# Kernel tuning notes

Hardware: AMD Instinct MI355X
Metric: run time of the kernel (lower is better)

## Reference

```python
import jax, jax.numpy as jnp
import numpy as np

# E2M1 (FP4) value table: low 3 bits magnitude, bit 3 sign (indices 8..15 negative)
FP4_TABLE = jnp.array([0.0, 0.5, 1.0, 1.5, 2.0, 3.0, 4.0, 6.0,
                       0.0, -0.5, -1.0, -1.5, -2.0, -3.0, -4.0, -6.0], dtype=jnp.float32)
FP4_BLOCK = 32  # per-row 1x32 scale groups


def dequant_fp4(packed, scale):
    """packed: [E, O, I//2] uint8 (two e2m1 nibbles per byte, low nibble first),
    scale: [E, O, I//32] float32 (e8m0, i.e. powers of two). Returns [E, O, I] float32."""
    lo = (packed & 15).astype(jnp.int32)
    hi = ((packed >> 4) & 15).astype(jnp.int32)
    # interleave low, high nibbles along the input dim (matches torch stack(...,-1).flatten)
    vals = FP4_TABLE[jnp.stack([lo, hi], axis=-1)]  # [E, O, I//2, 2]
    w = vals.reshape(packed.shape[0], packed.shape[1], packed.shape[2] * 2)
    return w * jnp.repeat(scale, FP4_BLOCK, axis=-1)


def setup_inputs() -> dict:
    T, H, F, E, K = 2048, 2048, 1024, 16, 4
    key = jax.random.key(0)
    k = jax.random.split(key, 8)
    hidden_states = jax.random.normal(k[0], (T, H), dtype=jnp.float32)
    topk_weights = jax.nn.softmax(jax.random.normal(k[1], (T, K)), axis=-1)
    topk_ids = jax.random.randint(k[2], (T, K), 0, E, dtype=jnp.int32)
    # checkpoint-native packed FP4 expert weights + e8m0 (power-of-two) scales
    gate_up_weight = jax.random.randint(k[3], (E, 2 * F, H // 2), 0, 256, dtype=jnp.int32).astype(jnp.uint8)
    gate_up_scale = jnp.exp2(jax.random.randint(k[4], (E, 2 * F, H // 32), -8, -5).astype(jnp.float32))
    down_weight = jax.random.randint(k[5], (E, H, F // 2), 0, 256, dtype=jnp.int32).astype(jnp.uint8)
    down_scale = jnp.exp2(jax.random.randint(k[6], (E, H, F // 32), -8, -5).astype(jnp.float32))
    return {"hidden_states": hidden_states, "topk_weights": topk_weights, "topk_ids": topk_ids,
            "gate_up_weight": gate_up_weight, "gate_up_scale": gate_up_scale,
            "down_weight": down_weight, "down_scale": down_scale}


def reference(hidden_states, topk_weights, topk_ids, gate_up_weight, gate_up_scale, down_weight, down_scale):
    # 1. dequantize checkpoint-native FP4 experts to dense float weights
    w_gate_up = dequant_fp4(gate_up_weight, gate_up_scale)  # [E, 2F, H]
    w_down = dequant_fp4(down_weight, down_scale)           # [E, H, F]
    T = hidden_states.shape[0]
    E = w_gate_up.shape[0]
    # 2. scatter routing weights into a dense [T, E] combine matrix
    combine = jnp.zeros((T, E), dtype=hidden_states.dtype)
    combine = combine.at[jnp.arange(T)[:, None], topk_ids].add(topk_weights)
    # 3. grouped expert GEMM (exact dense dispatch over experts)
    gu = jnp.einsum('th,eoh->teo', hidden_states, w_gate_up)  # [T, E, 2F]
    gate, up = jnp.split(gu, 2, axis=-1)                       # gate = first ffn_dim rows
    act = jax.nn.silu(gate) * up                               # SwiGLU (swiglu_limit=0 -> no clamping)
    act = act * combine[:, :, None]                            # fold routing weights into activations
    return jnp.einsum('tef,ehf->th', act, w_down)              # [T, H]
```

## Files before the change

### kernel.cpp

```cpp
#include <hip/hip_runtime.h>
#include <stdint.h>

#define HD 2048
#define FD 1024
#define NE 16
#define NPAIR 8192
#define BM 256
#define MAXT 48
#define LDK 40

typedef short bf16x8 __attribute__((ext_vector_type(8)));
typedef float f32x4 __attribute__((ext_vector_type(4)));
typedef unsigned short u16;

static __device__ __forceinline__ u16 f2bf(float f) {
  uint32_t u = __float_as_uint(f);
  u += 0x7FFFu + ((u >> 16) & 1u);
  return (u16)(u >> 16);
}

struct DqTab { uint32_t hA, hB, lA, lB; };

static __device__ __forceinline__ DqTab make_tab(uint32_t sbits) {
  int n = (int)(sbits >> 23) - 127;
  int q = n >> 1;
  uint32_t r = (uint32_t)(n & 1);
  uint32_t mq = (uint32_t)(-q);
  uint32_t sub1 = mq * 0x01010100u;
  uint32_t subA = mq * 0x01010101u;
  DqTab t;
  t.hA = (r ? 0x40403F00u : 0x3F3F3F00u) - sub1;
  t.hB = (r ? 0x41414040u : 0x40404040u) - subA;
  t.lA = r ? 0x40008000u : 0xC0800000u;
  t.lB = r ? 0x4000C080u : 0xC0804000u;
  return t;
}

static __device__ __forceinline__ void dq8(uint32_t p, const DqTab& t, uint32_t* d) {
  uint32_t a = p & 0x0F0F0F0Fu;
  uint32_t b = (p >> 4) & 0x0F0F0F0Fu;
  uint32_t x0 = __builtin_amdgcn_perm(b, a, 0x05010400u);
  uint32_t x1 = __builtin_amdgcn_perm(b, a, 0x07030602u);
  uint32_t m0 = x0 & 0x07070707u;
  uint32_t m1 = x1 & 0x07070707u;
  uint32_t h0 = __builtin_amdgcn_perm(t.hB, t.hA, m0) | ((x0 & 0x08080808u) << 4);
  uint32_t h1 = __builtin_amdgcn_perm(t.hB, t.hA, m1) | ((x1 & 0x08080808u) << 4);
  uint32_t l0 = __builtin_amdgcn_perm(t.lB, t.lA, m0);
  uint32_t l1 = __builtin_amdgcn_perm(t.lB, t.lA, m1);
  d[0] = __builtin_amdgcn_perm(h0, l0, 0x05010400u);
  d[1] = __builtin_amdgcn_perm(h0, l0, 0x07030602u);
  d[2] = __builtin_amdgcn_perm(h1, l1, 0x05010400u);
  d[3] = __builtin_amdgcn_perm(h1, l1, 0x07030602u);
}

static __device__ __forceinline__ uint32_t pack4(int4 v) {
  return (uint32_t)(v.x & 0xFF) | ((uint32_t)(v.y & 0xFF) << 8) |
         ((uint32_t)(v.z & 0xFF) << 16) | ((uint32_t)v.w << 24);
}

static __device__ __forceinline__ bf16x8 dqfrag(const uint32_t* pB, const uint32_t* pS,
                                                int row, int kkloc, int q) {
  uint32_t pb = pB[row * 17 + kkloc * 4 + q];
  DqTab t = make_tab(pS[row * 4 + kkloc]);
  uint32_t d[4];
  dq8(pb, t, d);
  union { uint32_t u[4]; bf16x8 v; } cv;
  cv.u[0] = d[0]; cv.u[1] = d[1]; cv.u[2] = d[2]; cv.u[3] = d[3];
  return cv.v;
}

__global__ void cast_kernel(const float* __restrict__ x, u16* __restrict__ xb) {
  int i = blockIdx.x * 256 + threadIdx.x;
  float4 v = ((const float4*)x)[i];
  ushort4 o;
  o.x = f2bf(v.x); o.y = f2bf(v.y); o.z = f2bf(v.z); o.w = f2bf(v.w);
  ((ushort4*)xb)[i] = o;
}

__global__ void zero_kernel(float4* __restrict__ out) {
  out[blockIdx.x * 256 + threadIdx.x] = float4{0.f, 0.f, 0.f, 0.f};
}

__global__ void route_kernel(const int* __restrict__ ids, const float* __restrict__ tw,
                             int* __restrict__ rows, float* __restrict__ rw,
                             int* __restrict__ te, int* __restrict__ pidx) {
  __shared__ int cnt[NE], base[NE], run[NE];
  int tid = threadIdx.x;
  if (tid < NE) { cnt[tid] = 0; run[tid] = 0; }
  __syncthreads();
  for (int i = tid; i < NPAIR; i += 256) atomicAdd(&cnt[ids[i]], 1);
  __syncthreads();
  if (tid == 0) {
    int cum = 0;
    for (int e = 0; e < NE; ++e) {
      base[e] = cum;
      int nt = (cnt[e] + BM - 1) >> 8;
      for (int j = 0; j < nt; ++j) te[(cum >> 8) + j] = e;
      cum += nt << 8;
    }
    for (int t = cum >> 8; t < MAXT; ++t) te[t] = -1;
  }
  __syncthreads();
  for (int i = tid; i < MAXT * BM; i += 256) {
    rows[i] = -1;
    rw[i] = 0.f;
    if (pidx) pidx[i] = -1;
  }
  __syncthreads();
  for (int i = tid; i < NPAIR; i += 256) {
    int e = ids[i];
    int p = base[e] + atomicAdd(&run[e], 1);
    rows[p] = i >> 2;
    rw[p] = tw[i];
    if (pidx) pidx[p] = i;
  }
}

__global__ __launch_bounds__(256, 2) void gemm1_kernel(
    const u16* __restrict__ xb, const int* __restrict__ gup32,
    const uint32_t* __restrict__ gus, const int* __restrict__ rows,
    const float* __restrict__ rw, const int* __restrict__ te,
    u16* __restrict__ act) {
  const int tile = blockIdx.y;
  const int e = te[tile];
  if (e < 0) return;
  const int f0 = blockIdx.x * 64;

  __shared__ u16 sA[2][BM * LDK];
  __shared__ uint32_t sBp[2][128 * 17];
  __shared__ uint32_t sSc[2][128 * 4];
  __shared__ int rows_s[BM];
  __shared__ float rw_s[BM];

  const int tid = threadIdx.x;
  rows_s[tid] = rows[tile * BM + tid];
  rw_s[tid] = rw[tile * BM + tid];
  __syncthreads();

  const int sr4 = tid >> 2, sg4 = tid & 3;
  uint32_t aof[4];
  int lofsAr[4];
#pragma unroll
  for (int r = 0; r < 4; ++r) {
    int rr = rows_s[sr4 + r * 64];
    rr = rr < 0 ? 0 : rr;
    aof[r] = (uint32_t)rr * HD + sg4 * 8;
    lofsAr[r] = (sr4 + r * 64) * LDK + sg4 * 8;
  }

  const int srow = tid >> 4;
  const int sseg = tid & 15;
  const int* gb = gup32 + (size_t)(e * 2048 + f0 + srow) * 1024 + sseg * 4;
  const int trow = tid >> 1;
  const int tpair = (tid & 1) * 2;
  const int to = trow < 64 ? f0 + trow : 1024 + f0 + (trow - 64);
  const uint32_t* scb = gus + (size_t)(e * 2048 + to) * 64 + tpair;

  const int lane = tid & 63;
  const int w = tid >> 6;
  const int q = lane >> 4, c = lane & 15;

  f32x4 Cg[4][4], Cu[4][4];
#pragma unroll
  for (int s = 0; s < 4; ++s)
#pragma unroll
    for (int t2 = 0; t2 < 4; ++t2) {
      Cg[s][t2] = f32x4{0.f, 0.f, 0.f, 0.f};
      Cu[s][t2] = f32x4{0.f, 0.f, 0.f, 0.f};
    }

  int4 breg[8];
  uint2 sreg;

  {
#pragma unroll
    for (int pp = 0; pp < 8; ++pp)
      breg[pp] = *(const int4*)(gb + (pp < 4 ? 0 : 983040) + pp * 16384);
    sreg = *(const uint2*)scb;
    uint4 a[4];
#pragma unroll
    for (int r = 0; r < 4; ++r) a[r] = *(const uint4*)(xb + aof[r]);
#pragma unroll
    for (int pp = 0; pp < 8; ++pp)
      sBp[0][(srow + pp * 16) * 17 + sseg] = pack4(breg[pp]);
    sSc[0][trow * 4 + tpair] = sreg.x;
    sSc[0][trow * 4 + tpair + 1] = sreg.y;
#pragma unroll
    for (int r = 0; r < 4; ++r) *(uint4*)&sA[0][lofsAr[r]] = a[r];
  }

  for (int kk = 0; kk < 64; ++kk) {
    const int p = kk & 1;
    const int sb = (kk >> 2) & 1;
    const int kkloc = kk & 3;
    __syncthreads();

    uint4 na[4];
    if (kk < 63) {
#pragma unroll
      for (int r = 0; r < 4; ++r)
        na[r] = *(const uint4*)(xb + aof[r] + (kk + 1) * 32);
    }
    if (kkloc == 0 && kk + 4 < 64) {
      const int boff = ((kk >> 2) + 1) * 64;
#pragma unroll
      for (int pp = 0; pp < 8; ++pp)
        breg[pp] = *(const int4*)(gb + boff + (pp < 4 ? 0 : 983040) + pp * 16384);
      sreg = *(const uint2*)(scb + ((kk >> 2) + 1) * 4);
    }

    bf16x8 af[4];
#pragma unroll
    for (int s = 0; s < 4; ++s)
      af[s] = *(const bf16x8*)&sA[p][(w * 64 + s * 16 + c) * LDK + q * 8];

#pragma unroll
    for (int t2 = 0; t2 < 4; ++t2) {
      bf16x8 bg = dqfrag(sBp[sb], sSc[sb], t2 * 16 + c, kkloc, q);
      bf16x8 bu = dqfrag(sBp[sb], sSc[sb], 64 + t2 * 16 + c, kkloc, q);
#pragma unroll
      for (int s = 0; s < 4; ++s) {
        Cg[s][t2] = __builtin_amdgcn_mfma_f32_16x16x32_bf16(af[s], bg, Cg[s][t2], 0, 0, 0);
        Cu[s][t2] = __builtin_amdgcn_mfma_f32_16x16x32_bf16(af[s], bu, Cu[s][t2], 0, 0, 0);
      }
    }

    if (kk < 63) {
#pragma unroll
      for (int r = 0; r < 4; ++r) *(uint4*)&sA[p ^ 1][lofsAr[r]] = na[r];
    }
    if (kkloc == 3 && kk < 63) {
      const int sbn = sb ^ 1;
#pragma unroll
      for (int pp = 0; pp < 8; ++pp)
        sBp[sbn][(srow + pp * 16) * 17 + sseg] = pack4(breg[pp]);
      sSc[sbn][trow * 4 + tpair] = sreg.x;
      sSc[sbn][trow * 4 + tpair + 1] = sreg.y;
    }
  }

#pragma unroll
  for (int s = 0; s < 4; ++s) {
    const int mlb = w * 64 + s * 16 + q * 4;
#pragma unroll
    for (int t2 = 0; t2 < 4; ++t2) {
      const int fg = f0 + t2 * 16 + c;
#pragma unroll
      for (int r = 0; r < 4; ++r) {
        const int ml = mlb + r;
        float g = Cg[s][t2][r];
        float u = Cu[s][t2][r];
        float aval = g / (1.f + __expf(-g)) * u * rw_s[ml];
        act[(size_t)(tile * BM + ml) * FD + fg] = f2bf(aval);
      }
    }
  }
}

__global__ __launch_bounds__(256, 2) void gemm2_kernel(
    const u16* __restrict__ act, const int* __restrict__ dwn32,
    const uint32_t* __restrict__ dsc, const int* __restrict__ rows,
    const int* __restrict__ pidx, const int* __restrict__ te,
    float* __restrict__ out, float* __restrict__ pout) {
  const int tile = blockIdx.y;
  const int e = te[tile];
  if (e < 0) return;
  const int h0 = blockIdx.x * 128;

  __shared__ u16 sA[2][BM * LDK];
  __shared__ uint32_t sBp[2][128 * 17];
  __shared__ uint32_t sSc[2][128 * 4];
  __shared__ int rows_s[BM];
  __shared__ int pidx_s[BM];

  const int tid = threadIdx.x;
  rows_s[tid] = rows[tile * BM + tid];
  pidx_s[tid] = pout ? pidx[tile * BM + tid] : -1;
  __syncthreads();

  const int sr4 = tid >> 2, sg4 = tid & 3;
  uint32_t aof[4];
  int lofsAr[4];
#pragma unroll
  for (int r = 0; r < 4; ++r) {
    aof[r] = (uint32_t)(tile * BM + sr4 + r * 64) * FD + sg4 * 8;
    lofsAr[r] = (sr4 + r * 64) * LDK + sg4 * 8;
  }

  const int srow = tid >> 4;
  const int sseg = tid & 15;
  const int* gb = dwn32 + (size_t)(e * 2048 + h0 + srow) * 512 + sseg * 4;
  const int trow = tid >> 1;
  const int tpair = (tid & 1) * 2;
  const uint32_t* scb = dsc + (size_t)(e * 2048 + h0 + trow) * 32 + tpair;

  const int lane = tid & 63;
  const int w = tid >> 6;
  const int q = lane >> 4, c = lane & 15;

  f32x4 Cd[4][8];
#pragma unroll
  for (int s = 0; s < 4; ++s)
#pragma unroll
    for (int t2 = 0; t2 < 8; ++t2) Cd[s][t2] = f32x4{0.f, 0.f, 0.f, 0.f};

  int4 breg[8];
  uint2 sreg;

  {
#pragma unroll
    for (int pp = 0; pp < 8; ++pp)
      breg[pp] = *(const int4*)(gb + pp * 8192);
    sreg = *(const uint2*)scb;
    uint4 a[4];
#pragma unroll
    for (int r = 0; r < 4; ++r) a[r] = *(const uint4*)(act + aof[r]);
#pragma unroll
    for (int pp = 0; pp < 8; ++pp)
      sBp[0][(srow + pp * 16) * 17 + sseg] = pack4(breg[pp]);
    sSc[0][trow * 4 + tpair] = sreg.x;
    sSc[0][trow * 4 + tpair + 1] = sreg.y;
#pragma unroll
    for (int r = 0; r < 4; ++r) *(uint4*)&sA[0][lofsAr[r]] = a[r];
  }

  for (int kk = 0; kk < 32; ++kk) {
    const int p = kk & 1;
    const int sb = (kk >> 2) & 1;
    const int kkloc = kk & 3;
    __syncthreads();

    uint4 na[4];
    if (kk < 31) {
#pragma unroll
      for (int r = 0; r < 4; ++r)
        na[r] = *(const uint4*)(act + aof[r] + (kk + 1) * 32);
    }
    if (kkloc == 0 && kk + 4 < 32) {
      const int boff = ((kk >> 2) + 1) * 64;
#pragma unroll
      for (int pp = 0; pp < 8; ++pp)
        breg[pp] = *(const int4*)(gb + boff + pp * 8192);
      sreg = *(const uint2*)(scb + ((kk >> 2) + 1) * 4);
    }

    bf16x8 af[4];
#pragma unroll
    for (int s = 0; s < 4; ++s)
      af[s] = *(const bf16x8*)&sA[p][(w * 64 + s * 16 + c) * LDK + q * 8];

#pragma unroll
    for (int t2 = 0; t2 < 8; ++t2) {
      bf16x8 bf_ = dqfrag(sBp[sb], sSc[sb], t2 * 16 + c, kkloc, q);
#pragma unroll
      for (int s = 0; s < 4; ++s)
        Cd[s][t2] = __builtin_amdgcn_mfma_f32_16x16x32_bf16(af[s], bf_, Cd[s][t2], 0, 0, 0);
    }

    if (kk < 31) {
#pragma unroll
      for (int r = 0; r < 4; ++r) *(uint4*)&sA[p ^ 1][lofsAr[r]] = na[r];
    }
    if (kkloc == 3 && kk < 31) {
      const int sbn = sb ^ 1;
#pragma unroll
      for (int pp = 0; pp < 8; ++pp)
        sBp[sbn][(srow + pp * 16) * 17 + sseg] = pack4(breg[pp]);
      sSc[sbn][trow * 4 + tpair] = sreg.x;
      sSc[sbn][trow * 4 + tpair + 1] = sreg.y;
    }
  }

  if (pout) {
#pragma unroll
    for (int s = 0; s < 4; ++s) {
      const int mlb = w * 64 + s * 16 + q * 4;
#pragma unroll
      for (int t2 = 0; t2 < 8; ++t2) {
        const int hg = h0 + t2 * 16 + c;
#pragma unroll
        for (int r = 0; r < 4; ++r) {
          int prow = pidx_s[mlb + r];
          if (prow >= 0) pout[(size_t)prow * HD + hg] = Cd[s][t2][r];
        }
      }
    }
  } else {
#pragma unroll
    for (int s = 0; s < 4; ++s) {
      const int mlb = w * 64 + s * 16 + q * 4;
#pragma unroll
      for (int t2 = 0; t2 < 8; ++t2) {
        const int hg = h0 + t2 * 16 + c;
#pragma unroll
        for (int r = 0; r < 4; ++r) {
          int token = rows_s[mlb + r];
          if (token >= 0) atomicAdd(&out[(size_t)token * HD + hg], Cd[s][t2][r]);
        }
      }
    }
  }
}

__global__ void finalize_kernel(const float4* __restrict__ pout, float4* __restrict__ out) {
  int j = blockIdx.x * 256 + threadIdx.x;
  int token = j >> 9;
  int col = j & 511;
  const float4* p = pout + ((size_t)token * 4) * 512 + col;
  float4 a = p[0], b = p[512], c = p[1024], d = p[1536];
  out[j] = float4{a.x + b.x + c.x + d.x, a.y + b.y + c.y + d.y,
                  a.z + b.z + c.z + d.z, a.w + b.w + c.w + d.w};
}

extern "C" void kernel_launch(void* const* d_in, const int* in_sizes, int n_in,
                              void* d_out, int out_size, void* d_ws, size_t ws_size,
                              hipStream_t stream) {
  const float* hidden = (const float*)d_in[0];
  const float* tw = (const float*)d_in[1];
  const int* ids = (const int*)d_in[2];
  const int* gup32 = (const int*)d_in[3];
  const uint32_t* gus = (const uint32_t*)d_in[4];
  const int* dwn32 = (const int*)d_in[5];
  const uint32_t* dsc = (const uint32_t*)d_in[6];
  float* out = (float*)d_out;

  char* ws = (char*)d_ws;
  int* rows = (int*)(ws);
  float* rw = (float*)(ws + 49152);
  int* te = (int*)(ws + 98304);
  u16* xb = (u16*)(ws + 131072);
  u16* act = (u16*)(ws + 8519680);

  const size_t POUT_OFF = 33685504ULL;
  const size_t PIDX_OFF = POUT_OFF + (size_t)NPAIR * HD * 4;
  const size_t WS_NEED = PIDX_OFF + (size_t)MAXT * BM * 4;
  const bool big = ws_size >= WS_NEED;
  float* pout = big ? (float*)(ws + POUT_OFF) : nullptr;
  int* pidx = big ? (int*)(ws + PIDX_OFF) : nullptr;

  cast_kernel<<<dim3(4096), dim3(256), 0, stream>>>(hidden, xb);
  if (!big) zero_kernel<<<dim3(4096), dim3(256), 0, stream>>>((float4*)out);
  route_kernel<<<dim3(1), dim3(256), 0, stream>>>(ids, tw, rows, rw, te, pidx);
  gemm1_kernel<<<dim3(16, MAXT), dim3(256), 0, stream>>>(xb, gup32, gus, rows, rw, te, act);
  gemm2_kernel<<<dim3(16, MAXT), dim3(256), 0, stream>>>(act, dwn32, dsc, rows, pidx, te, out, pout);
  if (big) finalize_kernel<<<dim3(1024 * 1024 / 256), dim3(256), 0, stream>>>((const float4*)pout, (float4*)out);
}
```

Before: 541.3 us.

## Load A tiles via global_load_lds with XOR swizzle and 64-wide K steps

```diff
diff --git a/kernel.cpp b/kernel.cpp
--- a/kernel.cpp
+++ b/kernel.cpp
@@ -7,7 +7,6 @@
 #define NPAIR 8192
 #define BM 256
 #define MAXT 48
-#define LDK 40
 
 typedef short bf16x8 __attribute__((ext_vector_type(8)));
 typedef float f32x4 __attribute__((ext_vector_type(4)));
@@ -59,14 +58,20 @@
 }
 
 static __device__ __forceinline__ bf16x8 dqfrag(const uint32_t* pB, const uint32_t* pS,
-                                                int row, int kkloc, int q) {
-  uint32_t pb = pB[row * 17 + kkloc * 4 + q];
-  DqTab t = make_tab(pS[row * 4 + kkloc]);
+                                                int row, int j, int q) {
+  uint32_t pb = pB[row * 9 + j * 4 + q];
+  DqTab t = make_tab(pS[row * 2 + j]);
   uint32_t d[4];
   dq8(pb, t, d);
   union { uint32_t u[4]; bf16x8 v; } cv;
   cv.u[0] = d[0]; cv.u[1] = d[1]; cv.u[2] = d[2]; cv.u[3] = d[3];
   return cv.v;
+}
+
+static __device__ __forceinline__ void glds16(const void* g, void* l) {
+  __builtin_amdgcn_global_load_lds(
+      (const __attribute__((address_space(1))) uint32_t*)g,
+      (__attribute__((address_space(3))) uint32_t*)l, 16, 0, 0);
 }
 
 __global__ void cast_kernel(const float* __restrict__ x, u16* __restrict__ xb) {
@@ -126,9 +131,9 @@
   if (e < 0) return;
   const int f0 = blockIdx.x * 64;
 
-  __shared__ u16 sA[2][BM * LDK];
-  __shared__ uint32_t sBp[2][128 * 17];
-  __shared__ uint32_t sSc[2][128 * 4];
+  __shared__ u16 sA[2][BM * 64];
+  __shared__ uint32_t sBp[2][128 * 9];
+  __shared__ uint32_t sSc[2][256];
   __shared__ int rows_s[BM];
   __shared__ float rw_s[BM];
 
@@ -137,29 +142,33 @@
   rw_s[tid] = rw[tile * BM + tid];
   __syncthreads();
 
-  const int sr4 = tid >> 2, sg4 = tid & 3;
-  uint32_t aof[4];
-  int lofsAr[4];
-#pragma unroll
-  for (int r = 0; r < 4; ++r) {
-    int rr = rows_s[sr4 + r * 64];
-    rr = rr < 0 ? 0 : rr;
-    aof[r] = (uint32_t)rr * HD + sg4 * 8;
-    lofsAr[r] = (sr4 + r * 64) * LDK + sg4 * 8;
-  }
-
-  const int srow = tid >> 4;
-  const int sseg = tid & 15;
-  const int* gb = gup32 + (size_t)(e * 2048 + f0 + srow) * 1024 + sseg * 4;
-  const int trow = tid >> 1;
-  const int tpair = (tid & 1) * 2;
-  const int to = trow < 64 ? f0 + trow : 1024 + f0 + (trow - 64);
-  const uint32_t* scb = gus + (size_t)(e * 2048 + to) * 64 + tpair;
-
   const int lane = tid & 63;
   const int w = tid >> 6;
   const int q = lane >> 4, c = lane & 15;
 
+  uint32_t aofs[8];
+#pragma unroll
+  for (int i = 0; i < 8; ++i) {
+    const int lrow = w * 64 + i * 8 + (lane >> 3);
+    int grow = rows_s[lrow];
+    grow = grow < 0 ? 0 : grow;
+    aofs[i] = (uint32_t)grow * HD + (uint32_t)(((lane & 7) ^ (lrow & 7)) << 3);
+  }
+
+  uint32_t obj[4];
+#pragma unroll
+  for (int j = 0; j < 4; ++j) {
+    const int r_ = (tid >> 3) + j * 32;
+    const int o_ = r_ < 64 ? f0 + r_ : 1024 + f0 + (r_ - 64);
+    obj[j] = (uint32_t)(e * 2048 + o_) * 1024 + (uint32_t)((tid & 7) << 2);
+  }
+  const int r_sc = tid >> 1;
+  const int o_sc = r_sc < 64 ? f0 + r_sc : 1024 + f0 + (r_sc - 64);
+  const uint32_t scb = (uint32_t)(e * 2048 + o_sc) * 64 + (uint32_t)(tid & 1);
+
+  const int x0 = ((q * 16) ^ ((c & 7) << 4)) >> 1;
+  const int x1 = ((64 + q * 16) ^ ((c & 7) << 4)) >> 1;
+
   f32x4 Cg[4][4], Cu[4][4];
 #pragma unroll
   for (int s = 0; s < 4; ++s)
@@ -169,74 +178,63 @@
       Cu[s][t2] = f32x4{0.f, 0.f, 0.f, 0.f};
     }
 
-  int4 breg[8];
-  uint2 sreg;
+  int4 breg[4];
+  uint32_t sreg;
 
   {
 #pragma unroll
-    for (int pp = 0; pp < 8; ++pp)
-      breg[pp] = *(const int4*)(gb + (pp < 4 ? 0 : 983040) + pp * 16384);
-    sreg = *(const uint2*)scb;
-    uint4 a[4];
-#pragma unroll
-    for (int r = 0; r < 4; ++r) a[r] = *(const uint4*)(xb + aof[r]);
-#pragma unroll
-    for (int pp = 0; pp < 8; ++pp)
-      sBp[0][(srow + pp * 16) * 17 + sseg] = pack4(breg[pp]);
-    sSc[0][trow * 4 + tpair] = sreg.x;
-    sSc[0][trow * 4 + tpair + 1] = sreg.y;
-#pragma unroll
-    for (int r = 0; r < 4; ++r) *(uint4*)&sA[0][lofsAr[r]] = a[r];
-  }
-
-  for (int kk = 0; kk < 64; ++kk) {
-    const int p = kk & 1;
-    const int sb = (kk >> 2) & 1;
-    const int kkloc = kk & 3;
+    for (int i = 0; i < 8; ++i)
+      glds16(xb + aofs[i], &sA[0][(w * 64 + i * 8) * 64]);
+    int4 b0[4];
+#pragma unroll
+    for (int j = 0; j < 4; ++j) b0[j] = *(const int4*)(gup32 + obj[j]);
+    uint32_t s0 = gus[scb];
+#pragma unroll
+    for (int j = 0; j < 4; ++j)
+      sBp[0][((tid >> 3) + j * 32) * 9 + (tid & 7)] = pack4(b0[j]);
+    sSc[0][tid] = s0;
+#pragma unroll
+    for (int j = 0; j < 4; ++j) breg[j] = *(const int4*)(gup32 + obj[j] + 32);
+    sreg = gus[scb + 2];
     __syncthreads();
-
-    uint4 na[4];
-    if (kk < 63) {
-#pragma unroll
-      for (int r = 0; r < 4; ++r)
-        na[r] = *(const uint4*)(xb + aof[r] + (kk + 1) * 32);
-    }
-    if (kkloc == 0 && kk + 4 < 64) {
-      const int boff = ((kk >> 2) + 1) * 64;
-#pragma unroll
-      for (int pp = 0; pp < 8; ++pp)
-        breg[pp] = *(const int4*)(gb + boff + (pp < 4 ? 0 : 983040) + pp * 16384);
-      sreg = *(const uint2*)(scb + ((kk >> 2) + 1) * 4);
-    }
-
-    bf16x8 af[4];
-#pragma unroll
-    for (int s = 0; s < 4; ++s)
-      af[s] = *(const bf16x8*)&sA[p][(w * 64 + s * 16 + c) * LDK + q * 8];
-
-#pragma unroll
-    for (int t2 = 0; t2 < 4; ++t2) {
-      bf16x8 bg = dqfrag(sBp[sb], sSc[sb], t2 * 16 + c, kkloc, q);
-      bf16x8 bu = dqfrag(sBp[sb], sSc[sb], 64 + t2 * 16 + c, kkloc, q);
-#pragma unroll
-      for (int s = 0; s < 4; ++s) {
-        Cg[s][t2] = __builtin_amdgcn_mfma_f32_16x16x32_bf16(af[s], bg, Cg[s][t2], 0, 0, 0);
-        Cu[s][t2] = __builtin_amdgcn_mfma_f32_16x16x32_bf16(af[s], bu, Cu[s][t2], 0, 0, 0);
+  }
+
+  for (int s = 0; s < 32; ++s) {
+    const int cur = s & 1;
+    if (s < 31) {
+#pragma unroll
+      for (int i = 0; i < 8; ++i)
+        glds16(xb + aofs[i] + (uint32_t)(s + 1) * 64, &sA[cur ^ 1][(w * 64 + i * 8) * 64]);
+#pragma unroll
+      for (int j = 0; j < 4; ++j)
+        sBp[cur ^ 1][((tid >> 3) + j * 32) * 9 + (tid & 7)] = pack4(breg[j]);
+      sSc[cur ^ 1][tid] = sreg;
+    }
+    if (s < 30) {
+#pragma unroll
+      for (int j = 0; j < 4; ++j)
+        breg[j] = *(const int4*)(gup32 + obj[j] + (uint32_t)(s + 2) * 32);
+      sreg = gus[scb + (uint32_t)(s + 2) * 2];
+    }
+#pragma unroll
+    for (int j = 0; j < 2; ++j) {
+      const int xo = j ? x1 : x0;
+      bf16x8 af[4];
+#pragma unroll
+      for (int s4 = 0; s4 < 4; ++s4)
+        af[s4] = *(const bf16x8*)&sA[cur][(w * 64 + s4 * 16 + c) * 64 + xo];
+#pragma unroll
+      for (int t2 = 0; t2 < 4; ++t2) {
+        bf16x8 bg = dqfrag(sBp[cur], sSc[cur], t2 * 16 + c, j, q);
+        bf16x8 bu = dqfrag(sBp[cur], sSc[cur], 64 + t2 * 16 + c, j, q);
+#pragma unroll
+        for (int s4 = 0; s4 < 4; ++s4) {
+          Cg[s4][t2] = __builtin_amdgcn_mfma_f32_16x16x32_bf16(af[s4], bg, Cg[s4][t2], 0, 0, 0);
+          Cu[s4][t2] = __builtin_amdgcn_mfma_f32_16x16x32_bf16(af[s4], bu, Cu[s4][t2], 0, 0, 0);
+        }
       }
     }
-
-    if (kk < 63) {
-#pragma unroll
-      for (int r = 0; r < 4; ++r) *(uint4*)&sA[p ^ 1][lofsAr[r]] = na[r];
-    }
-    if (kkloc == 3 && kk < 63) {
-      const int sbn = sb ^ 1;
-#pragma unroll
-      for (int pp = 0; pp < 8; ++pp)
-        sBp[sbn][(srow + pp * 16) * 17 + sseg] = pack4(breg[pp]);
-      sSc[sbn][trow * 4 + tpair] = sreg.x;
-      sSc[sbn][trow * 4 + tpair + 1] = sreg.y;
-    }
+    __syncthreads();
   }
 
 #pragma unroll
@@ -267,9 +265,9 @@
   if (e < 0) return;
   const int h0 = blockIdx.x * 128;
 
-  __shared__ u16 sA[2][BM * LDK];
-  __shared__ uint32_t sBp[2][128 * 17];
-  __shared__ uint32_t sSc[2][128 * 4];
+  __shared__ u16 sA[2][BM * 64];
+  __shared__ uint32_t sBp[2][128 * 9];
+  __shared__ uint32_t sSc[2][256];
   __shared__ int rows_s[BM];
   __shared__ int pidx_s[BM];
 
@@ -278,97 +276,88 @@
   pidx_s[tid] = pout ? pidx[tile * BM + tid] : -1;
   __syncthreads();
 
-  const int sr4 = tid >> 2, sg4 = tid & 3;
-  uint32_t aof[4];
-  int lofsAr[4];
-#pragma unroll
-  for (int r = 0; r < 4; ++r) {
-    aof[r] = (uint32_t)(tile * BM + sr4 + r * 64) * FD + sg4 * 8;
-    lofsAr[r] = (sr4 + r * 64) * LDK + sg4 * 8;
-  }
-
-  const int srow = tid >> 4;
-  const int sseg = tid & 15;
-  const int* gb = dwn32 + (size_t)(e * 2048 + h0 + srow) * 512 + sseg * 4;
-  const int trow = tid >> 1;
-  const int tpair = (tid & 1) * 2;
-  const uint32_t* scb = dsc + (size_t)(e * 2048 + h0 + trow) * 32 + tpair;
-
   const int lane = tid & 63;
   const int w = tid >> 6;
   const int q = lane >> 4, c = lane & 15;
 
+  uint32_t aofs[8];
+#pragma unroll
+  for (int i = 0; i < 8; ++i) {
+    const int lrow = w * 64 + i * 8 + (lane >> 3);
+    aofs[i] = (uint32_t)(tile * BM + lrow) * FD + (uint32_t)(((lane & 7) ^ (lrow & 7)) << 3);
+  }
+
+  uint32_t obj[4];
+#pragma unroll
+  for (int j = 0; j < 4; ++j) {
+    const int r_ = (tid >> 3) + j * 32;
+    obj[j] = (uint32_t)(e * 2048 + h0 + r_) * 512 + (uint32_t)((tid & 7) << 2);
+  }
+  const uint32_t scb = (uint32_t)(e * 2048 + h0 + (tid >> 1)) * 32 + (uint32_t)(tid & 1);
+
+  const int x0 = ((q * 16) ^ ((c & 7) << 4)) >> 1;
+  const int x1 = ((64 + q * 16) ^ ((c & 7) << 4)) >> 1;
+
   f32x4 Cd[4][8];
 #pragma unroll
   for (int s = 0; s < 4; ++s)
 #pragma unroll
     for (int t2 = 0; t2 < 8; ++t2) Cd[s][t2] = f32x4{0.f, 0.f, 0.f, 0.f};
 
-  int4 breg[8];
-  uint2 sreg;
+  int4 breg[4];
+  uint32_t sreg;
 
   {
 #pragma unroll
-    for (int pp = 0; pp < 8; ++pp)
-      breg[pp] = *(const int4*)(gb + pp * 8192);
-    sreg = *(const uint2*)scb;
-    uint4 a[4];
-#pragma unroll
-    for (int r = 0; r < 4; ++r) a[r] = *(const uint4*)(act + aof[r]);
-#pragma unroll
-    for (int pp = 0; pp < 8; ++pp)
-      sBp[0][(srow + pp * 16) * 17 + sseg] = pack4(breg[pp]);
-    sSc[0][trow * 4 + tpair] = sreg.x;
-    sSc[0][trow * 4 + tpair + 1] = sreg.y;
-#pragma unroll
-    for (int r = 0; r < 4; ++r) *(uint4*)&sA[0][lofsAr[r]] = a[r];
-  }
-
-  for (int kk = 0; kk < 32; ++kk) {
-    const int p = kk & 1;
-    const int sb = (kk >> 2) & 1;
-    const int kkloc = kk & 3;
+    for (int i = 0; i < 8; ++i)
+      glds16(act + aofs[i], &sA[0][(w * 64 + i * 8) * 64]);
+    int4 b0[4];
+#pragma unroll
+    for (int j = 0; j < 4; ++j) b0[j] = *(const int4*)(dwn32 + obj[j]);
+    uint32_t s0 = dsc[scb];
+#pragma unroll
+    for (int j = 0; j < 4; ++j)
+      sBp[0][((tid >> 3) + j * 32) * 9 + (tid & 7)] = pack4(b0[j]);
+    sSc[0][tid] = s0;
+#pragma unroll
+    for (int j = 0; j < 4; ++j) breg[j] = *(const int4*)(dwn32 + obj[j] + 32);
+    sreg = dsc[scb + 2];
     __syncthreads();
-
-    uint4 na[4];
-    if (kk < 31) {
-#pragma unroll
-      for (int r = 0; r < 4; ++r)
-        na[r] = *(const uint4*)(act + aof[r] + (kk + 1) * 32);
-    }
-    if (kkloc == 0 && kk + 4 < 32) {
-      const int boff = ((kk >> 2) + 1) * 64;
-#pragma unroll
-      for (int pp = 0; pp < 8; ++pp)
-        breg[pp] = *(const int4*)(gb + boff + pp * 8192);
-      sreg = *(const uint2*)(scb + ((kk >> 2) + 1) * 4);
-    }
-
-    bf16x8 af[4];
-#pragma unroll
-    for (int s = 0; s < 4; ++s)
-      af[s] = *(const bf16x8*)&sA[p][(w * 64 + s * 16 + c) * LDK + q * 8];
-
-#pragma unroll
-    for (int t2 = 0; t2 < 8; ++t2) {
-      bf16x8 bf_ = dqfrag(sBp[sb], sSc[sb], t2 * 16 + c, kkloc, q);
-#pragma unroll
-      for (int s = 0; s < 4; ++s)
-        Cd[s][t2] = __builtin_amdgcn_mfma_f32_16x16x32_bf16(af[s], bf_, Cd[s][t2], 0, 0, 0);
-    }
-
-    if (kk < 31) {
-#pragma unroll
-      for (int r = 0; r < 4; ++r) *(uint4*)&sA[p ^ 1][lofsAr[r]] = na[r];
-    }
-    if (kkloc == 3 && kk < 31) {
-      const int sbn = sb ^ 1;
-#pragma unroll
-      for (int pp = 0; pp < 8; ++pp)
-        sBp[sbn][(srow + pp * 16) * 17 + sseg] = pack4(breg[pp]);
-      sSc[sbn][trow * 4 + tpair] = sreg.x;
-      sSc[sbn][trow * 4 + tpair + 1] = sreg.y;
-    }
+  }
+
+  for (int s = 0; s < 16; ++s) {
+    const int cur = s & 1;
+    if (s < 15) {
+#pragma unroll
+      for (int i = 0; i < 8; ++i)
+        glds16(act + aofs[i] + (uint32_t)(s + 1) * 64, &sA[cur ^ 1][(w * 64 + i * 8) * 64]);
+#pragma unroll
+      for (int j = 0; j < 4; ++j)
+        sBp[cur ^ 1][((tid >> 3) + j * 32) * 9 + (tid & 7)] = pack4(breg[j]);
+      sSc[cur ^ 1][tid] = sreg;
+    }
+    if (s < 14) {
+#pragma unroll
+      for (int j = 0; j < 4; ++j)
+        breg[j] = *(const int4*)(dwn32 + obj[j] + (uint32_t)(s + 2) * 32);
+      sreg = dsc[scb + (uint32_t)(s + 2) * 2];
+    }
+#pragma unroll
+    for (int j = 0; j < 2; ++j) {
+      const int xo = j ? x1 : x0;
+      bf16x8 af[4];
+#pragma unroll
+      for (int s4 = 0; s4 < 4; ++s4)
+        af[s4] = *(const bf16x8*)&sA[cur][(w * 64 + s4 * 16 + c) * 64 + xo];
+#pragma unroll
+      for (int t2 = 0; t2 < 8; ++t2) {
+        bf16x8 bf_ = dqfrag(sBp[cur], sSc[cur], t2 * 16 + c, j, q);
+#pragma unroll
+        for (int s4 = 0; s4 < 4; ++s4)
+          Cd[s4][t2] = __builtin_amdgcn_mfma_f32_16x16x32_bf16(af[s4], bf_, Cd[s4][t2], 0, 0, 0);
+      }
+    }
+    __syncthreads();
   }
 
   if (pout) {
```

Measured after the change: 539.2 us. Within noise of the previous version (-0.4%).
